# Optimization experiments

Hardware: AMD Instinct MI355X
Metric: run time of the kernel (lower is better)

## Reference

```python
import jax, jax.numpy as jnp
import numpy as np

EPS = 1e-5  # equinox LayerNorm default eps

def setup_inputs() -> dict:
    key = jax.random.key(0)
    k1, k2, k3, k4, k5 = jax.random.split(key, 5)
    heads, d, dH, N = 16, 1024, 64, 2048
    # lecun-normal-ish scaling for fan_in=d
    s = 1.0 / np.sqrt(d)
    return {
        "x": jax.random.normal(k1, (d, N), dtype=jnp.float32),
        "WQ": jax.random.normal(k2, (heads, d, dH), dtype=jnp.float32) * s,
        "WK": jax.random.normal(k3, (heads, d, dH), dtype=jnp.float32) * s,
        "WV": jax.random.normal(k4, (heads, d, dH), dtype=jnp.float32) * s,
        "W0": jax.random.normal(k5, (d, d), dtype=jnp.float32) * s,
    }

def reference(x, WQ, WK, WV, W0):
    # x: [d, N]
    residual = x
    # equinox LayerNorm over full shape (d, N), no affine params
    mean = jnp.mean(x)
    var = jnp.var(x)
    xn = (x - mean) * jax.lax.rsqrt(var + EPS)
    # project: [h, d_model, dH] x [d_model, N] -> [h, dH, N]
    Q = jnp.einsum('hcd,ci->hdi', WQ, xn)
    K = jnp.einsum('hcd,ci->hdi', WK, xn)
    V = jnp.einsum('hcd,ci->hdi', WV, xn)
    dH = WK.shape[-1]
    dot = jnp.einsum('hdi,hdj->hij', Q, K)  # [h, N, N]
    alpha = jax.nn.softmax(dot / jnp.sqrt(jnp.asarray(dH, dot.dtype)), axis=-1)
    attn = jnp.einsum('hij,hdj->hdi', alpha, V)  # [h, dH, N]
    N = attn.shape[2]
    attn = attn.reshape(-1, N)  # [d, N]
    out = W0 @ attn
    return out + residual
```

## Files before the change

kernel.cpp:

```cpp
#include <hip/hip_runtime.h>
#include <math.h>

typedef unsigned short u16;
typedef _Float16 f16;
typedef __attribute__((ext_vector_type(8))) short bf16x8;
typedef __attribute__((ext_vector_type(4))) float f32x4;
typedef __attribute__((ext_vector_type(4))) f16 f16x4;

#define D_MODEL 1024
#define SEQ_N   2048
#define HEADS   16
#define DHEAD   64
#define M3      3072
#define NIT     (SEQ_N / 64)
#define QSCALE  0.18033688011112042f
#define EXPOFF  5.770780163555854f

#define GLOBAL_AS __attribute__((address_space(1)))
#define LDS_AS    __attribute__((address_space(3)))
#define ASYNC16(gp, lp) __builtin_amdgcn_global_load_lds( \
    (const GLOBAL_AS unsigned int*)(gp), (LDS_AS unsigned int*)(lp), 16, 0, 0)

__device__ __forceinline__ u16 f2bf(float f) {
  union { float f; unsigned int u; } v; v.f = f;
  unsigned int r = v.u + 0x7fffu + ((v.u >> 16) & 1u);
  return (u16)(r >> 16);
}

__global__ __launch_bounds__(256) void prep(const float* __restrict__ x,
                                            double* __restrict__ part,
                                            const float* __restrict__ WQ,
                                            const float* __restrict__ WK,
                                            const float* __restrict__ WV,
                                            const float* __restrict__ W0,
                                            u16* __restrict__ Wp,
                                            u16* __restrict__ W0p) {
  __shared__ double ls[256], lss[256];
  __shared__ float tile[32][65];
  int t = threadIdx.x;
  int b = blockIdx.x;
  if (b < 256) {
    const float4* x4 = (const float4*)x;
    const int n4 = (D_MODEL * SEQ_N) / 4;
    double s = 0.0, ss = 0.0;
    for (int idx = b * 256 + t; idx < n4; idx += 256 * 256) {
      float4 v = x4[idx];
      s  += (double)v.x + (double)v.y + (double)v.z + (double)v.w;
      ss += (double)v.x * v.x + (double)v.y * v.y + (double)v.z * v.z + (double)v.w * v.w;
    }
    ls[t] = s; lss[t] = ss;
    __syncthreads();
    for (int off = 128; off > 0; off >>= 1) {
      if (t < off) { ls[t] += ls[t + off]; lss[t] += lss[t + off]; }
      __syncthreads();
    }
    if (t == 0) { part[2 * b] = ls[0]; part[2 * b + 1] = lss[0]; }
    return;
  }
  int f = b - 256;
  int z = f >> 9;
  int rem = f & 511;
  if (z == 3) {
    int idx = rem * 512 + t;
#pragma unroll
    for (int r = 0; r < 2; ++r, idx += 256) {
      float4 v = ((const float4*)W0)[idx];
      unsigned int lo = (unsigned int)f2bf(v.x) | ((unsigned int)f2bf(v.y) << 16);
      unsigned int hi = (unsigned int)f2bf(v.z) | ((unsigned int)f2bf(v.w) << 16);
      uint2 o; o.x = lo; o.y = hi;
      *(uint2*)(&W0p[(size_t)idx * 4]) = o;
    }
    return;
  }
  const float* W = (z == 0) ? WQ : ((z == 1) ? WK : WV);
  int h = rem >> 5, cb = (rem & 31) * 32;
  int dh = t & 63, cl = t >> 6;
  for (int r = 0; r < 8; ++r) {
    int c = cl + r * 4;
    tile[c][dh] = W[((size_t)h * D_MODEL + cb + c) * DHEAD + dh];
  }
  __syncthreads();
  int c2 = t & 31, d2 = t >> 5;
  for (int r = 0; r < 8; ++r) {
    int dd = d2 + r * 8;
    Wp[(size_t)((z * HEADS + h) * DHEAD + dd) * D_MODEL + cb + c2] = f2bf(tile[c2][dd]);
  }
}

__global__ __launch_bounds__(256) void ln_norm_t(const float* __restrict__ x,
                                                 const double* __restrict__ part,
                                                 u16* __restrict__ xnt) {
  __shared__ double ls[256], lss[256];
  __shared__ float tile[64][65];
  int t = threadIdx.x;
  ls[t] = part[2 * t]; lss[t] = part[2 * t + 1];
  __syncthreads();
  for (int off = 128; off > 0; off >>= 1) {
    if (t < off) { ls[t] += ls[t + off]; lss[t] += lss[t + off]; }
    __syncthreads();
  }
  double inv = 1.0 / ((double)D_MODEL * (double)SEQ_N);
  double m = ls[0] * inv;
  double vv = lss[0] * inv - m * m;
  float mean = (float)m;
  float rstd = (float)(1.0 / sqrt(vv + 1e-5));

  int ib = blockIdx.x * 64, cb = blockIdx.y * 64;
  int il = t & 63, cl = t >> 6;
  for (int r = 0; r < 16; ++r) {
    int c = cl + r * 4;
    tile[c][il] = (x[(size_t)(cb + c) * SEQ_N + ib + il] - mean) * rstd;
  }
  __syncthreads();
  int c2 = t & 63, i2 = t >> 6;
  for (int r = 0; r < 16; ++r) {
    int i = i2 + r * 4;
    xnt[(size_t)(ib + i) * D_MODEL + cb + c2] = f2bf(tile[c2][i]);
  }
}

__global__ __launch_bounds__(256) void gemm_qkv(const u16* __restrict__ A,
                                                const u16* __restrict__ Bt,
                                                u16* __restrict__ Qt,
                                                u16* __restrict__ Kt,
                                                f16* __restrict__ Vb) {
  __shared__ __align__(16) u16 Alds[2 * 2 * 96 * 32];
  __shared__ __align__(16) u16 Blds[2 * 2 * 128 * 32];
  int t = threadIdx.x;
  int lane = t & 63, w = t >> 6;
  int g = lane >> 4, l16 = lane & 15;
  int wr = w >> 1, wc = w & 1;
  int flat = blockIdx.x;
  int wi = flat >> 3;
  int wx = wi & 7, wy = wi >> 3;
  int cx = (flat & 7) & 1, cy = (flat & 7) >> 1;
  int bx = cx * 8 + wx;
  int by = cy * 8 + wy;
  int mb = by * 96, nb = bx * 128;

  f32x4 acc[3][4];
#pragma unroll
  for (int i = 0; i < 3; ++i)
#pragma unroll
    for (int j = 0; j < 4; ++j) acc[i][j] = (f32x4){0.f, 0.f, 0.f, 0.f};

  const u16* AgP[3]; int ldsA[3];
#pragma unroll
  for (int r = 0; r < 3; ++r) {
    int idx = r * 256 + t;
    int kk = (idx >= 384) ? 1 : 0;
    int rem = idx - kk * 384;
    int row = rem >> 2, c4 = rem & 3;
    AgP[r] = A + (size_t)(mb + row) * D_MODEL + kk * 32 + c4 * 8;
    ldsA[r] = idx * 8;
  }
  const u16* BgP[4]; int ldsB[4];
#pragma unroll
  for (int r = 0; r < 4; ++r) {
    int idx = r * 256 + t;
    int kk = idx >> 9;
    int rem = idx & 511;
    int row = rem >> 2, c4 = rem & 3;
    BgP[r] = Bt + (size_t)(nb + row) * D_MODEL + kk * 32 + c4 * 8;
    ldsB[r] = idx * 8;
  }

#pragma unroll
  for (int r = 0; r < 3; ++r) ASYNC16(AgP[r], &Alds[ldsA[r]]);
#pragma unroll
  for (int r = 0; r < 4; ++r) ASYNC16(BgP[r], &Blds[ldsB[r]]);
#pragma unroll
  for (int r = 0; r < 3; ++r) ASYNC16(AgP[r] + 64, &Alds[6144 + ldsA[r]]);
#pragma unroll
  for (int r = 0; r < 4; ++r) ASYNC16(BgP[r] + 64, &Blds[8192 + ldsB[r]]);

  int cur = 0;
  for (int ks = 0; ks < 16; ++ks) {
    if (ks < 15) asm volatile("s_waitcnt vmcnt(7)" ::: "memory");
    else         asm volatile("s_waitcnt vmcnt(0)" ::: "memory");
    __builtin_amdgcn_s_barrier();
#pragma unroll
    for (int kk = 0; kk < 2; ++kk) {
      bf16x8 af[3], bf[4];
#pragma unroll
      for (int tm = 0; tm < 3; ++tm)
        af[tm] = *(const bf16x8*)(&Alds[cur * 6144 + kk * 3072 +
                                        (wr * 48 + tm * 16 + l16) * 32 + g * 8]);
#pragma unroll
      for (int tn = 0; tn < 4; ++tn)
        bf[tn] = *(const bf16x8*)(&Blds[cur * 8192 + kk * 4096 +
                                        (wc * 64 + tn * 16 + l16) * 32 + g * 8]);
#pragma unroll
      for (int tm = 0; tm < 3; ++tm)
#pragma unroll
        for (int tn = 0; tn < 4; ++tn)
          acc[tm][tn] = __builtin_amdgcn_mfma_f32_16x16x32_bf16(af[tm], bf[tn],
                                                                acc[tm][tn], 0, 0, 0);
    }
    __builtin_amdgcn_s_barrier();
    if (ks + 2 < 16) {
      int kb = (ks + 2) * 64;
#pragma unroll
      for (int r = 0; r < 3; ++r) ASYNC16(AgP[r] + kb, &Alds[cur * 6144 + ldsA[r]]);
#pragma unroll
      for (int r = 0; r < 4; ++r) ASYNC16(BgP[r] + kb, &Blds[cur * 8192 + ldsB[r]]);
    }
    cur ^= 1;
  }

#pragma unroll
  for (int tm = 0; tm < 3; ++tm) {
    int row0 = mb + wr * 48 + tm * 16 + g * 4;
#pragma unroll
    for (int tn = 0; tn < 4; ++tn) {
      int col = nb + wc * 64 + tn * 16 + l16;
      if (row0 < 2 * D_MODEL) {
        u16* T = (row0 < D_MODEL) ? Qt : Kt;
        float sc = (row0 < D_MODEL) ? QSCALE : 1.0f;
        int rbase = (row0 < D_MODEL) ? row0 : row0 - D_MODEL;
        ushort4 o;
        o.x = f2bf(acc[tm][tn][0] * sc); o.y = f2bf(acc[tm][tn][1] * sc);
        o.z = f2bf(acc[tm][tn][2] * sc); o.w = f2bf(acc[tm][tn][3] * sc);
        *(ushort4*)(&T[(size_t)col * D_MODEL + rbase]) = o;
      } else {
        int rbase = row0 - 2 * D_MODEL;
#pragma unroll
        for (int r = 0; r < 4; ++r)
          Vb[(size_t)(rbase + r) * SEQ_N + col] = (f16)acc[tm][tn][r];
      }
    }
  }
}

__global__ __launch_bounds__(256) void gemm_bf16(const u16* __restrict__ A,
                                                 const u16* __restrict__ Bt,
                                                 float* __restrict__ C,
                                                 const float* __restrict__ res,
                                                 int M, int N, int K) {
  __shared__ __align__(16) u16 Alds[2 * 2 * 64 * 32];
  __shared__ __align__(16) u16 Blds[2 * 2 * 64 * 32];
  int t = threadIdx.x;
  int w = t >> 6, lane = t & 63;
  int g = lane >> 4, l16 = lane & 15;
  int flat = blockIdx.x;
  int wi = flat >> 3;
  int wx = wi & 7, wy = wi >> 3;
  int cx = (flat & 7) & 3, cy = (flat & 7) >> 2;
  int bx = cx * 8 + wx;
  int by = cy * 8 + wy;
  int mb = by * 64, nb = bx * 64;
  f32x4 acc[4];
  for (int i = 0; i < 4; ++i) acc[i] = (f32x4){0.f, 0.f, 0.f, 0.f};

  const u16* AgP[2]; const u16* BgP[2]; int ldsO[2];
#pragma unroll
  for (int r = 0; r < 2; ++r) {
    int idx = r * 256 + t;
    int kk = idx >> 8;
    int rem = idx & 255;
    int row = rem >> 2, c4 = rem & 3;
    AgP[r] = A + (size_t)(mb + row) * K + kk * 32 + c4 * 8;
    BgP[r] = Bt + (size_t)(nb + row) * K + kk * 32 + c4 * 8;
    ldsO[r] = idx * 8;
  }

#pragma unroll
  for (int r = 0; r < 2; ++r) { ASYNC16(AgP[r], &Alds[ldsO[r]]); ASYNC16(BgP[r], &Blds[ldsO[r]]); }
#pragma unroll
  for (int r = 0; r < 2; ++r) {
    ASYNC16(AgP[r] + 64, &Alds[4096 + ldsO[r]]);
    ASYNC16(BgP[r] + 64, &Blds[4096 + ldsO[r]]);
  }

  int cur = 0;
  const int NK = 16;
  for (int ks = 0; ks < NK; ++ks) {
    if (ks < NK - 1) asm volatile("s_waitcnt vmcnt(4)" ::: "memory");
    else             asm volatile("s_waitcnt vmcnt(0)" ::: "memory");
    __builtin_amdgcn_s_barrier();
#pragma unroll
    for (int kk = 0; kk < 2; ++kk) {
      bf16x8 af = *(const bf16x8*)(&Alds[cur * 4096 + kk * 2048 + (w * 16 + l16) * 32 + g * 8]);
#pragma unroll
      for (int tn = 0; tn < 4; ++tn) {
        bf16x8 bf = *(const bf16x8*)(&Blds[cur * 4096 + kk * 2048 + (tn * 16 + l16) * 32 + g * 8]);
        acc[tn] = __builtin_amdgcn_mfma_f32_16x16x32_bf16(af, bf, acc[tn], 0, 0, 0);
      }
    }
    __builtin_amdgcn_s_barrier();
    if (ks + 2 < NK) {
      int kb = (ks + 2) * 64;
#pragma unroll
      for (int r = 0; r < 2; ++r) {
        ASYNC16(AgP[r] + kb, &Alds[cur * 4096 + ldsO[r]]);
        ASYNC16(BgP[r] + kb, &Blds[cur * 4096 + ldsO[r]]);
      }
    }
    cur ^= 1;
  }
  int col0 = nb + l16;
  int row0 = mb + w * 16 + g * 4;
#pragma unroll
  for (int tn = 0; tn < 4; ++tn) {
    int col = col0 + tn * 16;
#pragma unroll
    for (int r = 0; r < 4; ++r) {
      int row = row0 + r;
      float v = acc[tn][r];
      if (res) v += res[(size_t)row * N + col];
      C[(size_t)row * N + col] = v;
    }
  }
}

__global__ __launch_bounds__(256, 2) void attn_mfma(const u16* __restrict__ Qt,
                                                    const u16* __restrict__ Kt,
                                                    const f16* __restrict__ Vb,
                                                    u16* __restrict__ attnt) {
  __shared__ __align__(16) u16 Klds[2][64][72];
  __shared__ __align__(16) f16 Vlds[2][64][72];
  int flat = blockIdx.x;
  int xcd = flat & 7, idx = flat >> 3;
  int h  = xcd * 2 + (idx >> 5);
  int ib = (idx & 31) * 64;
  int t = threadIdx.x;
  int w = t >> 6, lane = t & 63;
  int g = lane >> 4, l16 = lane & 15;

  bf16x8 bq[2];
  {
    const u16* qb = Qt + (size_t)(ib + w * 16 + l16) * D_MODEL + h * DHEAD + g * 8;
    bq[0] = *(const bf16x8*)(qb);
    bq[1] = *(const bf16x8*)(qb + 32);
  }

  f32x4 acc_o[4];
#pragma unroll
  for (int i = 0; i < 4; ++i) acc_o[i] = (f32x4){0.f, 0.f, 0.f, 0.f};
  f32x4 acc_l = (f32x4){0.f, 0.f, 0.f, 0.f};
  f16x4 ones;
  ones[0] = (f16)1.f; ones[1] = (f16)1.f; ones[2] = (f16)1.f; ones[3] = (f16)1.f;

  int srow = t >> 2, sc0 = (t & 3) * 16;
  const u16* Kg = Kt + (size_t)srow * D_MODEL + h * DHEAD + sc0;
  const f16* Vg = Vb + (size_t)(h * DHEAD + srow) * SEQ_N + sc0;

  uint4 ka = *(const uint4*)(Kg);
  uint4 kb = *(const uint4*)(Kg + 8);
  uint4 va = *(const uint4*)(Vg);
  uint4 vb = *(const uint4*)(Vg + 8);
  *(uint4*)(&Klds[0][srow][sc0]) = ka;
  *(uint4*)(&Klds[0][srow][sc0 + 8]) = kb;
  *(uint4*)(&Vlds[0][srow][sc0]) = va;
  *(uint4*)(&Vlds[0][srow][sc0 + 8]) = vb;
  __syncthreads();

  int cur = 0;
  for (int it = 0; it < NIT; ++it) {
    if (it + 1 < NIT) {
      const u16* Kn = Kg + (size_t)(it + 1) * 64 * D_MODEL;
      const f16* Vn = Vg + (it + 1) * 64;
      ka = *(const uint4*)(Kn);
      kb = *(const uint4*)(Kn + 8);
      va = *(const uint4*)(Vn);
      vb = *(const uint4*)(Vn + 8);
    }

    f32x4 s[4];
#pragma unroll
    for (int i = 0; i < 4; ++i) s[i] = (f32x4){0.f, 0.f, 0.f, 0.f};
    __builtin_amdgcn_s_setprio(1);
#pragma unroll
    for (int kk = 0; kk < 2; ++kk)
#pragma unroll
      for (int tn = 0; tn < 4; ++tn) {
        bf16x8 ak = *(const bf16x8*)(&Klds[cur][tn * 16 + l16][kk * 32 + g * 8]);
        s[tn] = __builtin_amdgcn_mfma_f32_16x16x32_bf16(ak, bq[kk], s[tn], 0, 0, 0);
      }
    __builtin_amdgcn_s_setprio(0);
    f16x4 pf[4];
#pragma unroll
    for (int tn = 0; tn < 4; ++tn) {
      f16x4 p;
#pragma unroll
      for (int r = 0; r < 4; ++r)
        p[r] = (f16)exp2f(s[tn][r] - EXPOFF);
      pf[tn] = p;
    }
    __builtin_amdgcn_s_setprio(1);
#pragma unroll
    for (int tn = 0; tn < 4; ++tn) {
      acc_l = __builtin_amdgcn_mfma_f32_16x16x16f16(pf[tn], ones, acc_l, 0, 0, 0);
#pragma unroll
      for (int td = 0; td < 4; ++td) {
        f16x4 bv = *(const f16x4*)(&Vlds[cur][td * 16 + l16][tn * 16 + g * 4]);
        acc_o[td] =
            __builtin_amdgcn_mfma_f32_16x16x16f16(pf[tn], bv, acc_o[td], 0, 0, 0);
      }
    }
    __builtin_amdgcn_s_setprio(0);

    if (it + 1 < NIT) {
      *(uint4*)(&Klds[cur ^ 1][srow][sc0]) = ka;
      *(uint4*)(&Klds[cur ^ 1][srow][sc0 + 8]) = kb;
      *(uint4*)(&Vlds[cur ^ 1][srow][sc0]) = va;
      *(uint4*)(&Vlds[cur ^ 1][srow][sc0 + 8]) = vb;
    }
    __syncthreads();
    cur ^= 1;
  }

  float inv0 = 1.0f / acc_l[0];
  float inv1 = 1.0f / acc_l[1];
  float inv2 = 1.0f / acc_l[2];
  float inv3 = 1.0f / acc_l[3];
#pragma unroll
  for (int td = 0; td < 4; ++td) {
    int dh = h * DHEAD + td * 16 + l16;
    int i0 = ib + w * 16 + g * 4;
    attnt[(size_t)(i0 + 0) * D_MODEL + dh] = f2bf(acc_o[td][0] * inv0);
    attnt[(size_t)(i0 + 1) * D_MODEL + dh] = f2bf(acc_o[td][1] * inv1);
    attnt[(size_t)(i0 + 2) * D_MODEL + dh] = f2bf(acc_o[td][2] * inv2);
    attnt[(size_t)(i0 + 3) * D_MODEL + dh] = f2bf(acc_o[td][3] * inv3);
  }
}

extern "C" void kernel_launch(void* const* d_in, const int* in_sizes, int n_in,
                              void* d_out, int out_size, void* d_ws, size_t ws_size,
                              hipStream_t stream) {
  const float* x  = (const float*)d_in[0];
  const float* WQ = (const float*)d_in[1];
  const float* WK = (const float*)d_in[2];
  const float* WV = (const float*)d_in[3];
  const float* W0 = (const float*)d_in[4];
  float* out = (float*)d_out;

  char* ws = (char*)d_ws;
  size_t off = 0;
  double* part  = (double*)(ws + off); off += 8192;
  u16*    xnt   = (u16*)(ws + off); off += (size_t)SEQ_N * D_MODEL * 2;
  u16*    Wp    = (u16*)(ws + off); off += (size_t)M3 * D_MODEL * 2;
  u16*    W0p   = (u16*)(ws + off); off += (size_t)D_MODEL * D_MODEL * 2;
  u16*    Qt    = (u16*)(ws + off); off += (size_t)SEQ_N * D_MODEL * 2;
  u16*    Kt    = (u16*)(ws + off); off += (size_t)SEQ_N * D_MODEL * 2;
  f16*    Vb    = (f16*)(ws + off); off += (size_t)D_MODEL * SEQ_N * 2;
  u16*    attnt = (u16*)(ws + off); off += (size_t)SEQ_N * D_MODEL * 2;

  prep<<<256 + 2048, 256, 0, stream>>>(x, part, WQ, WK, WV, W0, Wp, W0p);
  ln_norm_t<<<dim3(SEQ_N / 64, D_MODEL / 64), 256, 0, stream>>>(x, part, xnt);
  gemm_qkv<<<512, 256, 0, stream>>>(Wp, xnt, Qt, Kt, Vb);
  attn_mfma<<<512, 256, 0, stream>>>(Qt, Kt, Vb, attnt);
  gemm_bf16<<<512, 256, 0, stream>>>(W0p, attnt, out, x, D_MODEL, SEQ_N, D_MODEL);
}
```

Measured before the change: 153.1 us.

## XOR-swizzle LDS tiles in GEMM and attention kernels to avoid bank conflicts

Applies an XOR swizzle to the 16-byte chunk index in the LDS layouts of both GEMM kernels. The swizzle is applied on the global-source side of the async global-to-LDS loads and matched on the fragment reads. The attention kernel drops its padded 72-wide K/V tiles for unpadded 64-wide tiles with a row-based XOR swizzle. The aim is fewer LDS bank conflicts on the MFMA fragment reads and less shared memory use, at the cost of extra index arithmetic. Gather-style global addressing could also weaken load coalescing slightly.

Measured after the change: 153.5 us. No clear change (+0.2%).

```diff
diff --git a/kernel.cpp b/kernel.cpp
--- a/kernel.cpp
+++ b/kernel.cpp
@@ -151,7 +151,8 @@
     int kk = (idx >= 384) ? 1 : 0;
     int rem = idx - kk * 384;
     int row = rem >> 2, c4 = rem & 3;
-    AgP[r] = A + (size_t)(mb + row) * D_MODEL + kk * 32 + c4 * 8;
+    int csw = c4 ^ ((row >> 1) & 3);
+    AgP[r] = A + (size_t)(mb + row) * D_MODEL + kk * 32 + csw * 8;
     ldsA[r] = idx * 8;
   }
   const u16* BgP[4]; int ldsB[4];
@@ -161,7 +162,8 @@
     int kk = idx >> 9;
     int rem = idx & 511;
     int row = rem >> 2, c4 = rem & 3;
-    BgP[r] = Bt + (size_t)(nb + row) * D_MODEL + kk * 32 + c4 * 8;
+    int csw = c4 ^ ((row >> 1) & 3);
+    BgP[r] = Bt + (size_t)(nb + row) * D_MODEL + kk * 32 + csw * 8;
     ldsB[r] = idx * 8;
   }
 
@@ -174,6 +176,7 @@
 #pragma unroll
   for (int r = 0; r < 4; ++r) ASYNC16(BgP[r] + 64, &Blds[8192 + ldsB[r]]);
 
+  int rowa0 = wr * 48, rowb0 = wc * 64;
   int cur = 0;
   for (int ks = 0; ks < 16; ++ks) {
     if (ks < 15) asm volatile("s_waitcnt vmcnt(7)" ::: "memory");
@@ -183,13 +186,17 @@
     for (int kk = 0; kk < 2; ++kk) {
       bf16x8 af[3], bf[4];
 #pragma unroll
-      for (int tm = 0; tm < 3; ++tm)
-        af[tm] = *(const bf16x8*)(&Alds[cur * 6144 + kk * 3072 +
-                                        (wr * 48 + tm * 16 + l16) * 32 + g * 8]);
-#pragma unroll
-      for (int tn = 0; tn < 4; ++tn)
-        bf[tn] = *(const bf16x8*)(&Blds[cur * 8192 + kk * 4096 +
-                                        (wc * 64 + tn * 16 + l16) * 32 + g * 8]);
+      for (int tm = 0; tm < 3; ++tm) {
+        int row = rowa0 + tm * 16 + l16;
+        int gs = g ^ ((row >> 1) & 3);
+        af[tm] = *(const bf16x8*)(&Alds[cur * 6144 + kk * 3072 + row * 32 + gs * 8]);
+      }
+#pragma unroll
+      for (int tn = 0; tn < 4; ++tn) {
+        int row = rowb0 + tn * 16 + l16;
+        int gs = g ^ ((row >> 1) & 3);
+        bf[tn] = *(const bf16x8*)(&Blds[cur * 8192 + kk * 4096 + row * 32 + gs * 8]);
+      }
 #pragma unroll
       for (int tm = 0; tm < 3; ++tm)
 #pragma unroll
@@ -259,8 +266,9 @@
     int kk = idx >> 8;
     int rem = idx & 255;
     int row = rem >> 2, c4 = rem & 3;
-    AgP[r] = A + (size_t)(mb + row) * K + kk * 32 + c4 * 8;
-    BgP[r] = Bt + (size_t)(nb + row) * K + kk * 32 + c4 * 8;
+    int csw = c4 ^ ((row >> 1) & 3);
+    AgP[r] = A + (size_t)(mb + row) * K + kk * 32 + csw * 8;
+    BgP[r] = Bt + (size_t)(nb + row) * K + kk * 32 + csw * 8;
     ldsO[r] = idx * 8;
   }
 
@@ -280,10 +288,14 @@
     __builtin_amdgcn_s_barrier();
 #pragma unroll
     for (int kk = 0; kk < 2; ++kk) {
-      bf16x8 af = *(const bf16x8*)(&Alds[cur * 4096 + kk * 2048 + (w * 16 + l16) * 32 + g * 8]);
+      int rowa = w * 16 + l16;
+      int gsa = g ^ ((rowa >> 1) & 3);
+      bf16x8 af = *(const bf16x8*)(&Alds[cur * 4096 + kk * 2048 + rowa * 32 + gsa * 8]);
 #pragma unroll
       for (int tn = 0; tn < 4; ++tn) {
-        bf16x8 bf = *(const bf16x8*)(&Blds[cur * 4096 + kk * 2048 + (tn * 16 + l16) * 32 + g * 8]);
+        int rowb = tn * 16 + l16;
+        int gsb = g ^ ((rowb >> 1) & 3);
+        bf16x8 bf = *(const bf16x8*)(&Blds[cur * 4096 + kk * 2048 + rowb * 32 + gsb * 8]);
         acc[tn] = __builtin_amdgcn_mfma_f32_16x16x32_bf16(af, bf, acc[tn], 0, 0, 0);
       }
     }
@@ -313,12 +325,13 @@
   }
 }
 
+#define KSW(buf_, row_, ch_) ((buf_)*4096 + (row_)*64 + ((((ch_) ^ ((row_)&7)))*8))
 __global__ __launch_bounds__(256, 2) void attn_mfma(const u16* __restrict__ Qt,
                                                     const u16* __restrict__ Kt,
                                                     const f16* __restrict__ Vb,
                                                     u16* __restrict__ attnt) {
-  __shared__ __align__(16) u16 Klds[2][64][72];
-  __shared__ __align__(16) f16 Vlds[2][64][72];
+  __shared__ __align__(16) u16 Klds[2 * 64 * 64];
+  __shared__ __align__(16) f16 Vlds[2 * 64 * 64];
   int flat = blockIdx.x;
   int xcd = flat & 7, idx = flat >> 3;
   int h  = xcd * 2 + (idx >> 5);
@@ -342,6 +355,7 @@
   ones[0] = (f16)1.f; ones[1] = (f16)1.f; ones[2] = (f16)1.f; ones[3] = (f16)1.f;
 
   int srow = t >> 2, sc0 = (t & 3) * 16;
+  int c0 = (t & 3) * 2;
   const u16* Kg = Kt + (size_t)srow * D_MODEL + h * DHEAD + sc0;
   const f16* Vg = Vb + (size_t)(h * DHEAD + srow) * SEQ_N + sc0;
 
@@ -349,10 +363,10 @@
   uint4 kb = *(const uint4*)(Kg + 8);
   uint4 va = *(const uint4*)(Vg);
   uint4 vb = *(const uint4*)(Vg + 8);
-  *(uint4*)(&Klds[0][srow][sc0]) = ka;
-  *(uint4*)(&Klds[0][srow][sc0 + 8]) = kb;
-  *(uint4*)(&Vlds[0][srow][sc0]) = va;
-  *(uint4*)(&Vlds[0][srow][sc0 + 8]) = vb;
+  *(uint4*)(&Klds[KSW(0, srow, c0)])     = ka;
+  *(uint4*)(&Klds[KSW(0, srow, c0 + 1)]) = kb;
+  *(uint4*)(&Vlds[KSW(0, srow, c0)])     = va;
+  *(uint4*)(&Vlds[KSW(0, srow, c0 + 1)]) = vb;
   __syncthreads();
 
   int cur = 0;
@@ -374,7 +388,8 @@
     for (int kk = 0; kk < 2; ++kk)
 #pragma unroll
       for (int tn = 0; tn < 4; ++tn) {
-        bf16x8 ak = *(const bf16x8*)(&Klds[cur][tn * 16 + l16][kk * 32 + g * 8]);
+        int row = tn * 16 + l16;
+        bf16x8 ak = *(const bf16x8*)(&Klds[KSW(cur, row, kk * 4 + g)]);
         s[tn] = __builtin_amdgcn_mfma_f32_16x16x32_bf16(ak, bq[kk], s[tn], 0, 0, 0);
       }
     __builtin_amdgcn_s_setprio(0);
@@ -393,7 +408,8 @@
       acc_l = __builtin_amdgcn_mfma_f32_16x16x16f16(pf[tn], ones, acc_l, 0, 0, 0);
 #pragma unroll
       for (int td = 0; td < 4; ++td) {
-        f16x4 bv = *(const f16x4*)(&Vlds[cur][td * 16 + l16][tn * 16 + g * 4]);
+        int row = td * 16 + l16;
+        f16x4 bv = *(const f16x4*)(&Vlds[KSW(cur, row, tn * 2 + (g >> 1)) + (g & 1) * 4]);
         acc_o[td] =
             __builtin_amdgcn_mfma_f32_16x16x16f16(pf[tn], bv, acc_o[td], 0, 0, 0);
       }
@@ -401,10 +417,10 @@
     __builtin_amdgcn_s_setprio(0);
 
     if (it + 1 < NIT) {
-      *(uint4*)(&Klds[cur ^ 1][srow][sc0]) = ka;
-      *(uint4*)(&Klds[cur ^ 1][srow][sc0 + 8]) = kb;
-      *(uint4*)(&Vlds[cur ^ 1][srow][sc0]) = va;
-      *(uint4*)(&Vlds[cur ^ 1][srow][sc0 + 8]) = vb;
+      *(uint4*)(&Klds[KSW(cur ^ 1, srow, c0)])     = ka;
+      *(uint4*)(&Klds[KSW(cur ^ 1, srow, c0 + 1)]) = kb;
+      *(uint4*)(&Vlds[KSW(cur ^ 1, srow, c0)])     = va;
+      *(uint4*)(&Vlds[KSW(cur ^ 1, srow, c0 + 1)]) = vb;
     }
     __syncthreads();
     cur ^= 1;
```
